# Kernel tuning notes

Hardware: AMD Instinct MI355X
Metric: run time of the kernel (lower is better)

The kernel has to match this reference:

```python
import jax, jax.numpy as jnp
import numpy as np

B, S, V, E, H = 512, 256, 128, 128, 512


def setup_inputs() -> dict:
    key = jax.random.key(0)
    ks = jax.random.split(key, 12)
    s = lambda k, shape, fan: jax.random.normal(k, shape, jnp.float32) * (1.0 / np.sqrt(fan))
    return {
        "x": jax.random.randint(ks[0], (B, S), 0, V),
        "emb": s(ks[1], (V, E), E),
        "Wih0": s(ks[2], (E, H), E),
        "bih0": s(ks[3], (H,), H),
        "Whh0": s(ks[4], (H, H), H),
        "bhh0": s(ks[5], (H,), H),
        "Wih1": s(ks[6], (H, H), H),
        "bih1": s(ks[7], (H,), H),
        "Whh1": s(ks[8], (H, H), H),
        "bhh1": s(ks[9], (H,), H),
        "Wout": s(ks[10], (H, V), H),
        "bout": s(ks[11], (V,), V),
    }


def reference(x, emb, Wih0, bih0, Whh0, bhh0, Wih1, bih1, Whh1, bhh1, Wout, bout):
    # x: [B,S] int -> embedded [B,S,E]
    embedded = emb[x]
    xs = jnp.transpose(embedded, (1, 0, 2))  # [S,B,E] for time-major scan
    h0 = jnp.zeros((x.shape[0], Whh0.shape[0]), embedded.dtype)
    h1 = jnp.zeros((x.shape[0], Whh1.shape[0]), embedded.dtype)

    def step(carry, x_t):
        h0, h1 = carry
        h0 = jnp.tanh(x_t @ Wih0 + bih0 + h0 @ Whh0 + bhh0)
        h1 = jnp.tanh(h0 @ Wih1 + bih1 + h1 @ Whh1 + bhh1)
        return (h0, h1), h1

    _, hs = jax.lax.scan(step, (h0, h1), xs)  # hs: [S,B,H]
    logits = jnp.einsum("sbh,hv->sbv", hs, Wout) + bout
    return jnp.transpose(logits, (1, 0, 2))  # [B,S,V]
```

## Files before the change

### kernel.cpp

```cpp
#include <hip/hip_runtime.h>
#include <hip/hip_bf16.h>


#define Bb 512
#define Ss 256
#define Vv 128
#define Ee 128
#define Hh 512

typedef _Float16 f16;
typedef __attribute__((ext_vector_type(8))) _Float16 f16x8;
typedef __attribute__((ext_vector_type(4))) float f32x4;

#define OFF_H0   0u
#define OFF_H1   2097152u
#define OFF_W0T  4194304u
#define OFF_W1T  4849664u
#define OFF_WOT  5898240u
#define OFF_EMB  6029312u
#define OFF_FLAG 6062080u
#define OFF_CTR  6063104u
#define WS_TOTAL 6063168u

__device__ __forceinline__ f16x8 ld8(const f16* p) {
    return *reinterpret_cast<const f16x8*>(p);
}
#define INV_L1() asm volatile("buffer_inv sc0" ::: "memory")
#define MFMA16(a, b, c) __builtin_amdgcn_mfma_f32_16x16x32_f16((a), (b), (c), 0, 0, 0)

__global__ void prep_kernel(const float* __restrict__ Wih0, const float* __restrict__ Whh0,
                            const float* __restrict__ Wih1, const float* __restrict__ Whh1,
                            const float* __restrict__ Wout, const float* __restrict__ emb,
                            char* __restrict__ ws)
{
    f16* w0t = (f16*)(ws + OFF_W0T);
    f16* w1t = (f16*)(ws + OFF_W1T);
    f16* wot = (f16*)(ws + OFF_WOT);
    f16* e16 = (f16*)(ws + OFF_EMB);
    const int N0 = 512 * 640, N1 = 512 * 1024, N2 = 128 * 512, NE = 128 * 128;
    int i = blockIdx.x * blockDim.x + threadIdx.x;
    if (i < N0) {
        int c = i / 640, k = i - c * 640;
        w0t[i] = (f16)((k < 128) ? Wih0[k * 512 + c] : Whh0[(k - 128) * 512 + c]);
    } else if (i < N0 + N1) {
        int j = i - N0;
        int c = j >> 10, k = j & 1023;
        w1t[j] = (f16)((k < 512) ? Wih1[k * 512 + c] : Whh1[(k - 512) * 512 + c]);
    } else if (i < N0 + N1 + N2) {
        int j = i - (N0 + N1);
        int v = j >> 9, k = j & 511;
        wot[j] = (f16)(Wout[k * 128 + v]);
    } else if (i < N0 + N1 + N2 + NE) {
        int j = i - (N0 + N1 + N2);
        e16[j] = (f16)(emb[j]);
    }
}

__global__ __launch_bounds__(512, 2)
void rnn_kernel(
    const int* __restrict__ x,
    const float* __restrict__ bih0, const float* __restrict__ bhh0,
    const float* __restrict__ bih1, const float* __restrict__ bhh1,
    const float* __restrict__ bout, float* __restrict__ out,
    f16* __restrict__ h0buf, f16* __restrict__ h1buf,
    const f16* __restrict__ w0t, const f16* __restrict__ w1t,
    const f16* __restrict__ wot, const f16* __restrict__ e16,
    int* __restrict__ flags, int* __restrict__ xcdctr)
{
    const int tid = threadIdx.x;

    __shared__ int sslot[2];
    if (tid == 0) {
        unsigned int xcc;
        asm volatile("s_getreg_b32 %0, hwreg(20, 0, 4)" : "=s"(xcc));
        int s = atomicAdd(&xcdctr[xcc & 15], 1);
        sslot[0] = (int)(xcc & 15);
        sslot[1] = s;
    }
    __syncthreads();
    const int xcd = sslot[0], slot = sslot[1];
    const int grp = xcd * 2 + (slot >> 4);
    const int sub = slot & 15;
    const int stg = sub >> 3;
    const int jc  = sub & 7;
    if (grp >= 16) return;
    const int row0 = grp * 32;
    const int col0 = jc * 64;

    int* gflags = flags + grp * 16;

    __shared__ int tok[32];
    __shared__ float bs[64];

    const int lane = tid & 63;
    const int wv = tid >> 6;
    const int mt = wv >> 2, nt = wv & 3;
    const int ar = lane & 15;
    const int kg8 = (lane >> 4) << 3;
    const int arow = row0 + mt * 16 + ar;
    const int crow = row0 + mt * 16 + ((lane >> 4) << 2);
    const int ccol = col0 + nt * 16 + ar;

    if (tid < 64) {
        bs[tid] = (stg == 0) ? (bih0[col0 + tid] + bhh0[col0 + tid])
                             : (bih1[col0 + tid] + bhh1[col0 + tid]);
    }
    __syncthreads();
    const float cbias = bs[nt * 16 + ar];

    if (stg == 0) {
        f16x8 bfr[20];
        {
            const f16* wp = w0t + ccol * 640 + kg8;
            #pragma unroll
            for (int kc = 0; kc < 20; ++kc) bfr[kc] = ld8(wp + kc * 32);
            #pragma unroll
            for (int kc = 0; kc < 20; ++kc) asm volatile("" : "+v"(bfr[kc]));
        }
        const int vcol = jc * 16 + ar;
        const float pbias = bout[vcol];
        const f16* pwb = wot + vcol * Hh + kg8;
        const int prow_base = row0 + mt * 16;

        for (int t = 0; t < Ss; ++t) {
            if (tid >= 64 && tid < 96) tok[tid - 64] = x[(row0 + tid - 64) * Ss + t];
            if (tid < 16) {
                const int tgt = (tid < 8) ? t : (t - 3);
                int it = 0;
                while (__hip_atomic_load(&gflags[tid], __ATOMIC_RELAXED, __HIP_MEMORY_SCOPE_AGENT) < tgt) {
                    if (++it > (1 << 18)) break;
                    __builtin_amdgcn_s_sleep(1);
                }
            }
            __syncthreads();
            INV_L1();
            f16x8 ef[4];
            const f16* ea = e16 + tok[mt * 16 + ar] * Ee + kg8;
            #pragma unroll
            for (int kc = 0; kc < 4; ++kc) ef[kc] = ld8(ea + kc * 32);
            f16x8 hf[16];
            const f16* ha = h0buf + ((t + 3) & 3) * (Bb * Hh) + arow * Hh + kg8;
            #pragma unroll
            for (int kc = 0; kc < 16; ++kc) hf[kc] = ld8(ha + kc * 32);
            f32x4 a0 = {0.f,0.f,0.f,0.f}, a1 = a0, a2 = a0, a3 = a0;
            a0 = MFMA16(ef[0], bfr[0], a0); a1 = MFMA16(ef[1], bfr[1], a1);
            a2 = MFMA16(ef[2], bfr[2], a2); a3 = MFMA16(ef[3], bfr[3], a3);
            #pragma unroll
            for (int kc = 0; kc < 16; kc += 4) {
                a0 = MFMA16(hf[kc + 0], bfr[4 + kc + 0], a0);
                a1 = MFMA16(hf[kc + 1], bfr[4 + kc + 1], a1);
                a2 = MFMA16(hf[kc + 2], bfr[4 + kc + 2], a2);
                a3 = MFMA16(hf[kc + 3], bfr[4 + kc + 3], a3);
            }
            f32x4 acc = (a0 + a1) + (a2 + a3);
            f16* ho = h0buf + (t & 3) * (Bb * Hh) + crow * Hh + ccol;
            #pragma unroll
            for (int i = 0; i < 4; ++i) ho[i * Hh] = (f16)(tanhf(acc[i] + cbias));
            if (t >= 4 && (wv & 3) == (t & 3)) {
                const int tp = t - 4;
                f16x8 pf[16];
                const f16* pa = h1buf + (tp & 3) * (Bb * Hh) + (prow_base + ar) * Hh + kg8;
                #pragma unroll
                for (int kc = 0; kc < 16; ++kc) pf[kc] = ld8(pa + kc * 32);
                f32x4 p0 = {0.f,0.f,0.f,0.f}, p1 = p0, p2 = p0, p3 = p0;
                #pragma unroll
                for (int kc = 0; kc < 16; kc += 4) {
                    p0 = MFMA16(pf[kc + 0], ld8(pwb + (kc + 0) * 32), p0);
                    p1 = MFMA16(pf[kc + 1], ld8(pwb + (kc + 1) * 32), p1);
                    p2 = MFMA16(pf[kc + 2], ld8(pwb + (kc + 2) * 32), p2);
                    p3 = MFMA16(pf[kc + 3], ld8(pwb + (kc + 3) * 32), p3);
                }
                f32x4 pr = (p0 + p1) + (p2 + p3);
                float* op = out + (size_t)(prow_base + ((lane >> 4) << 2)) * (Ss * Vv) + tp * Vv + vcol;
                #pragma unroll
                for (int i = 0; i < 4; ++i) op[i * (Ss * Vv)] = pr[i] + pbias;
            }
            __syncthreads();
            if (tid == 0)
                __hip_atomic_store(&gflags[jc], t + 1, __ATOMIC_RELAXED, __HIP_MEMORY_SCOPE_AGENT);
        }
        if (tid < 8) {
            int it = 0;
            while (__hip_atomic_load(&gflags[8 + tid], __ATOMIC_RELAXED, __HIP_MEMORY_SCOPE_AGENT) < Ss) {
                if (++it > (1 << 18)) break;
                __builtin_amdgcn_s_sleep(1);
            }
        }
        __syncthreads();
        INV_L1();
        {
            const int tp = 252 + (wv & 3);
            f16x8 pf[16];
            const f16* pa = h1buf + (tp & 3) * (Bb * Hh) + (prow_base + ar) * Hh + kg8;
            #pragma unroll
            for (int kc = 0; kc < 16; ++kc) pf[kc] = ld8(pa + kc * 32);
            f32x4 p0 = {0.f,0.f,0.f,0.f}, p1 = p0, p2 = p0, p3 = p0;
            #pragma unroll
            for (int kc = 0; kc < 16; kc += 4) {
                p0 = MFMA16(pf[kc + 0], ld8(pwb + (kc + 0) * 32), p0);
                p1 = MFMA16(pf[kc + 1], ld8(pwb + (kc + 1) * 32), p1);
                p2 = MFMA16(pf[kc + 2], ld8(pwb + (kc + 2) * 32), p2);
                p3 = MFMA16(pf[kc + 3], ld8(pwb + (kc + 3) * 32), p3);
            }
            f32x4 pr = (p0 + p1) + (p2 + p3);
            float* op = out + (size_t)(prow_base + ((lane >> 4) << 2)) * (Ss * Vv) + tp * Vv + vcol;
            #pragma unroll
            for (int i = 0; i < 4; ++i) op[i * (Ss * Vv)] = pr[i] + pbias;
        }
    } else {
        f16x8 bfr[32];
        {
            const f16* wp = w1t + ccol * 1024 + kg8;
            #pragma unroll
            for (int kc = 0; kc < 32; ++kc) bfr[kc] = ld8(wp + kc * 32);
            #pragma unroll
            for (int kc = 0; kc < 32; ++kc) asm volatile("" : "+v"(bfr[kc]));
        }
        for (int t = 0; t < Ss; ++t) {
            if (tid < 16) {
                const int tgt = (tid < 8) ? (t + 1) : t;
                int it = 0;
                while (__hip_atomic_load(&gflags[tid], __ATOMIC_RELAXED, __HIP_MEMORY_SCOPE_AGENT) < tgt) {
                    if (++it > (1 << 18)) break;
                    __builtin_amdgcn_s_sleep(1);
                }
            }
            __syncthreads();
            INV_L1();
            f32x4 a0 = {0.f,0.f,0.f,0.f}, a1 = a0, a2 = a0, a3 = a0;
            {
                f16x8 hf[16];
                const f16* h0a = h0buf + (t & 3) * (Bb * Hh) + arow * Hh + kg8;
                #pragma unroll
                for (int kc = 0; kc < 16; ++kc) hf[kc] = ld8(h0a + kc * 32);
                #pragma unroll
                for (int kc = 0; kc < 16; kc += 4) {
                    a0 = MFMA16(hf[kc + 0], bfr[kc + 0], a0);
                    a1 = MFMA16(hf[kc + 1], bfr[kc + 1], a1);
                    a2 = MFMA16(hf[kc + 2], bfr[kc + 2], a2);
                    a3 = MFMA16(hf[kc + 3], bfr[kc + 3], a3);
                }
            }
            {
                f16x8 hf[16];
                const f16* h1a = h1buf + ((t + 3) & 3) * (Bb * Hh) + arow * Hh + kg8;
                #pragma unroll
                for (int kc = 0; kc < 16; ++kc) hf[kc] = ld8(h1a + kc * 32);
                #pragma unroll
                for (int kc = 0; kc < 16; kc += 4) {
                    a0 = MFMA16(hf[kc + 0], bfr[16 + kc + 0], a0);
                    a1 = MFMA16(hf[kc + 1], bfr[16 + kc + 1], a1);
                    a2 = MFMA16(hf[kc + 2], bfr[16 + kc + 2], a2);
                    a3 = MFMA16(hf[kc + 3], bfr[16 + kc + 3], a3);
                }
            }
            f32x4 acc = (a0 + a1) + (a2 + a3);
            f16* ho = h1buf + (t & 3) * (Bb * Hh) + crow * Hh + ccol;
            #pragma unroll
            for (int i = 0; i < 4; ++i) ho[i * Hh] = (f16)(tanhf(acc[i] + cbias));
            __syncthreads();
            if (tid == 0)
                __hip_atomic_store(&gflags[8 + jc], t + 1, __ATOMIC_RELAXED, __HIP_MEMORY_SCOPE_AGENT);
        }
    }
}

extern "C" void kernel_launch(void* const* d_in, const int* in_sizes, int n_in,
                              void* d_out, int out_size, void* d_ws, size_t ws_size,
                              hipStream_t stream) {
    const int*   x    = (const int*)d_in[0];
    const float* emb  = (const float*)d_in[1];
    const float* Wih0 = (const float*)d_in[2];
    const float* bih0 = (const float*)d_in[3];
    const float* Whh0 = (const float*)d_in[4];
    const float* bhh0 = (const float*)d_in[5];
    const float* Wih1 = (const float*)d_in[6];
    const float* bih1 = (const float*)d_in[7];
    const float* Whh1 = (const float*)d_in[8];
    const float* bhh1 = (const float*)d_in[9];
    const float* Wout = (const float*)d_in[10];
    const float* bout = (const float*)d_in[11];
    float* out = (float*)d_out;
    char*  ws  = (char*)d_ws;

    hipMemsetAsync(d_ws, 0, WS_TOTAL, stream);

    {
        const int total = 512 * 640 + 512 * 1024 + 128 * 512 + 128 * 128;
        prep_kernel<<<(total + 1023) / 1024, 1024, 0, stream>>>(Wih0, Whh0, Wih1, Whh1, Wout, emb, ws);
    }

    f16* h0buf = (f16*)(ws + OFF_H0);
    f16* h1buf = (f16*)(ws + OFF_H1);
    f16* w0t   = (f16*)(ws + OFF_W0T);
    f16* w1t   = (f16*)(ws + OFF_W1T);
    f16* wot   = (f16*)(ws + OFF_WOT);
    f16* e16   = (f16*)(ws + OFF_EMB);
    int* flags = (int*)(ws + OFF_FLAG);
    int* ctr   = (int*)(ws + OFF_CTR);

    void* args[] = { (void*)&x, (void*)&bih0, (void*)&bhh0, (void*)&bih1, (void*)&bhh1,
                     (void*)&bout, (void*)&out, (void*)&h0buf, (void*)&h1buf,
                     (void*)&w0t, (void*)&w1t, (void*)&wot, (void*)&e16,
                     (void*)&flags, (void*)&ctr };
    hipLaunchCooperativeKernel((void*)rnn_kernel, dim3(256), dim3(512), args, 0, stream);
}
```

Before: 2.362 ms.

## Stage RNN weights in LDS and coalesce hidden-state writes via LDS staging

Moves the per-block weight slices (W0, W1, Wout, embedding table) from registers and global memory into padded LDS buffers that are read as MFMA fragments each step. Hidden-state outputs are first staged in LDS and then written to global memory as coalesced 8-byte atomic stores, followed by an explicit vmcnt wait before the flag is published. The L1 invalidate is changed to sc1 scope with a preceding wait. This frees registers (the occupancy hint drops to 1 block per CU) and cuts scattered 2-byte global stores, at the cost of LDS reads in the inner loop and an extra barrier per timestep.

```diff
diff --git a/kernel.cpp b/kernel.cpp
--- a/kernel.cpp
+++ b/kernel.cpp
@@ -22,10 +22,22 @@
 #define OFF_CTR  6063104u
 #define WS_TOTAL 6063168u
 
+#define L_WO   82944
+#define L_EMB  99584
+#define ST_W0  1296
+#define ST_WO  1040
+#define ST_EM  272
+#define ST_W1  2064
+#define L_HS   134400
+#define LDS_BYTES 138496
+
 __device__ __forceinline__ f16x8 ld8(const f16* p) {
     return *reinterpret_cast<const f16x8*>(p);
 }
-#define INV_L1() asm volatile("buffer_inv sc0" ::: "memory")
+__device__ __forceinline__ f16x8 lds_frag(const char* lds, int rowByte, int kElem) {
+    return *reinterpret_cast<const f16x8*>(lds + rowByte + kElem * 2);
+}
+#define INV_L1() asm volatile("s_waitcnt vmcnt(0)\n\tbuffer_inv sc1" ::: "memory")
 #define MFMA16(a, b, c) __builtin_amdgcn_mfma_f32_16x16x32_f16((a), (b), (c), 0, 0, 0)
 
 __global__ void prep_kernel(const float* __restrict__ Wih0, const float* __restrict__ Whh0,
@@ -56,7 +68,7 @@
     }
 }
 
-__global__ __launch_bounds__(512, 2)
+__global__ __launch_bounds__(512)
 void rnn_kernel(
     const int* __restrict__ x,
     const float* __restrict__ bih0, const float* __restrict__ bhh0,
@@ -67,9 +79,10 @@
     const f16* __restrict__ wot, const f16* __restrict__ e16,
     int* __restrict__ flags, int* __restrict__ xcdctr)
 {
+    static __shared__ __attribute__((aligned(16))) char lds[LDS_BYTES];
     const int tid = threadIdx.x;
 
-    __shared__ int sslot[2];
+    __shared__ __attribute__((aligned(16))) int sslot[4];
     if (tid == 0) {
         unsigned int xcc;
         asm volatile("s_getreg_b32 %0, hwreg(20, 0, 4)" : "=s"(xcc));
@@ -89,8 +102,8 @@
 
     int* gflags = flags + grp * 16;
 
-    __shared__ int tok[32];
-    __shared__ float bs[64];
+    __shared__ __attribute__((aligned(16))) int tok[32];
+    __shared__ __attribute__((aligned(16))) float bs[64];
 
     const int lane = tid & 63;
     const int wv = tid >> 6;
@@ -98,28 +111,41 @@
     const int ar = lane & 15;
     const int kg8 = (lane >> 4) << 3;
     const int arow = row0 + mt * 16 + ar;
-    const int crow = row0 + mt * 16 + ((lane >> 4) << 2);
-    const int ccol = col0 + nt * 16 + ar;
-
+    const int cB   = nt * 16 + ar;
+    const int rloc = mt * 16 + ((lane >> 4) << 2);
+
+    if (stg == 0) {
+        for (int i = tid; i < 5120; i += 512) {
+            int c = i / 80, kc = i - c * 80;
+            *(f16x8*)(lds + c * ST_W0 + kc * 16) = ld8(w0t + (col0 + c) * 640 + kc * 8);
+        }
+        for (int i = tid; i < 1024; i += 512) {
+            int r = i >> 6, kc = i & 63;
+            *(f16x8*)(lds + L_WO + r * ST_WO + kc * 16) = ld8(wot + (jc * 16 + r) * 512 + kc * 8);
+        }
+        for (int i = tid; i < 2048; i += 512) {
+            int r = i >> 4, kc = i & 15;
+            *(f16x8*)(lds + L_EMB + r * ST_EM + kc * 16) = ld8(e16 + r * 128 + kc * 8);
+        }
+    } else {
+        for (int i = tid; i < 8192; i += 512) {
+            int c = i >> 7, kc = i & 127;
+            *(f16x8*)(lds + c * ST_W1 + kc * 16) = ld8(w1t + (col0 + c) * 1024 + kc * 8);
+        }
+    }
     if (tid < 64) {
         bs[tid] = (stg == 0) ? (bih0[col0 + tid] + bhh0[col0 + tid])
                              : (bih1[col0 + tid] + bhh1[col0 + tid]);
     }
     __syncthreads();
-    const float cbias = bs[nt * 16 + ar];
+    const float cbias = bs[cB];
+    f16* hstg = (f16*)(lds + L_HS);
 
     if (stg == 0) {
-        f16x8 bfr[20];
-        {
-            const f16* wp = w0t + ccol * 640 + kg8;
-            #pragma unroll
-            for (int kc = 0; kc < 20; ++kc) bfr[kc] = ld8(wp + kc * 32);
-            #pragma unroll
-            for (int kc = 0; kc < 20; ++kc) asm volatile("" : "+v"(bfr[kc]));
-        }
+        const int w0Row = cB * ST_W0;
         const int vcol = jc * 16 + ar;
         const float pbias = bout[vcol];
-        const f16* pwb = wot + vcol * Hh + kg8;
+        const int woRow = L_WO + ar * ST_WO;
         const int prow_base = row0 + mt * 16;
 
         for (int t = 0; t < Ss; ++t) {
@@ -134,28 +160,33 @@
             }
             __syncthreads();
             INV_L1();
-            f16x8 ef[4];
-            const f16* ea = e16 + tok[mt * 16 + ar] * Ee + kg8;
-            #pragma unroll
-            for (int kc = 0; kc < 4; ++kc) ef[kc] = ld8(ea + kc * 32);
+            const int myTok = tok[mt * 16 + ar];
+            const int embRow = L_EMB + myTok * ST_EM;
             f16x8 hf[16];
             const f16* ha = h0buf + ((t + 3) & 3) * (Bb * Hh) + arow * Hh + kg8;
             #pragma unroll
             for (int kc = 0; kc < 16; ++kc) hf[kc] = ld8(ha + kc * 32);
             f32x4 a0 = {0.f,0.f,0.f,0.f}, a1 = a0, a2 = a0, a3 = a0;
-            a0 = MFMA16(ef[0], bfr[0], a0); a1 = MFMA16(ef[1], bfr[1], a1);
-            a2 = MFMA16(ef[2], bfr[2], a2); a3 = MFMA16(ef[3], bfr[3], a3);
-            #pragma unroll
-            for (int kc = 0; kc < 16; kc += 4) {
-                a0 = MFMA16(hf[kc + 0], bfr[4 + kc + 0], a0);
-                a1 = MFMA16(hf[kc + 1], bfr[4 + kc + 1], a1);
-                a2 = MFMA16(hf[kc + 2], bfr[4 + kc + 2], a2);
-                a3 = MFMA16(hf[kc + 3], bfr[4 + kc + 3], a3);
+            #pragma unroll
+            for (int kc = 0; kc < 4; ++kc) {
+                f16x8 af = lds_frag(lds, embRow, kc * 32 + kg8);
+                f16x8 bw = lds_frag(lds, w0Row, kc * 32 + kg8);
+                if ((kc & 3) == 0) a0 = MFMA16(af, bw, a0);
+                else if ((kc & 3) == 1) a1 = MFMA16(af, bw, a1);
+                else if ((kc & 3) == 2) a2 = MFMA16(af, bw, a2);
+                else a3 = MFMA16(af, bw, a3);
+            }
+            #pragma unroll
+            for (int kc = 0; kc < 16; ++kc) {
+                f16x8 bw = lds_frag(lds, w0Row, 128 + kc * 32 + kg8);
+                if ((kc & 3) == 0) a0 = MFMA16(hf[kc], bw, a0);
+                else if ((kc & 3) == 1) a1 = MFMA16(hf[kc], bw, a1);
+                else if ((kc & 3) == 2) a2 = MFMA16(hf[kc], bw, a2);
+                else a3 = MFMA16(hf[kc], bw, a3);
             }
             f32x4 acc = (a0 + a1) + (a2 + a3);
-            f16* ho = h0buf + (t & 3) * (Bb * Hh) + crow * Hh + ccol;
-            #pragma unroll
-            for (int i = 0; i < 4; ++i) ho[i * Hh] = (f16)(tanhf(acc[i] + cbias));
+            #pragma unroll
+            for (int i = 0; i < 4; ++i) hstg[(rloc + i) * 64 + cB] = (f16)(tanhf(acc[i] + cbias));
             if (t >= 4 && (wv & 3) == (t & 3)) {
                 const int tp = t - 4;
                 f16x8 pf[16];
@@ -165,16 +196,24 @@
                 f32x4 p0 = {0.f,0.f,0.f,0.f}, p1 = p0, p2 = p0, p3 = p0;
                 #pragma unroll
                 for (int kc = 0; kc < 16; kc += 4) {
-                    p0 = MFMA16(pf[kc + 0], ld8(pwb + (kc + 0) * 32), p0);
-                    p1 = MFMA16(pf[kc + 1], ld8(pwb + (kc + 1) * 32), p1);
-                    p2 = MFMA16(pf[kc + 2], ld8(pwb + (kc + 2) * 32), p2);
-                    p3 = MFMA16(pf[kc + 3], ld8(pwb + (kc + 3) * 32), p3);
+                    p0 = MFMA16(pf[kc + 0], lds_frag(lds, woRow, (kc + 0) * 32 + kg8), p0);
+                    p1 = MFMA16(pf[kc + 1], lds_frag(lds, woRow, (kc + 1) * 32 + kg8), p1);
+                    p2 = MFMA16(pf[kc + 2], lds_frag(lds, woRow, (kc + 2) * 32 + kg8), p2);
+                    p3 = MFMA16(pf[kc + 3], lds_frag(lds, woRow, (kc + 3) * 32 + kg8), p3);
                 }
                 f32x4 pr = (p0 + p1) + (p2 + p3);
                 float* op = out + (size_t)(prow_base + ((lane >> 4) << 2)) * (Ss * Vv) + tp * Vv + vcol;
                 #pragma unroll
                 for (int i = 0; i < 4; ++i) op[i * (Ss * Vv)] = pr[i] + pbias;
             }
+            __syncthreads();
+            {
+                unsigned long long v = ((const unsigned long long*)hstg)[tid];
+                unsigned long long* hg = (unsigned long long*)(h0buf + (t & 3) * (Bb * Hh)
+                                            + (row0 + (tid >> 4)) * Hh + col0 + ((tid & 15) << 2));
+                __hip_atomic_store(hg, v, __ATOMIC_RELAXED, __HIP_MEMORY_SCOPE_AGENT);
+            }
+            asm volatile("s_waitcnt vmcnt(0)" ::: "memory");
             __syncthreads();
             if (tid == 0)
                 __hip_atomic_store(&gflags[jc], t + 1, __ATOMIC_RELAXED, __HIP_MEMORY_SCOPE_AGENT);
@@ -197,10 +236,10 @@
             f32x4 p0 = {0.f,0.f,0.f,0.f}, p1 = p0, p2 = p0, p3 = p0;
             #pragma unroll
             for (int kc = 0; kc < 16; kc += 4) {
-                p0 = MFMA16(pf[kc + 0], ld8(pwb + (kc + 0) * 32), p0);
-                p1 = MFMA16(pf[kc + 1], ld8(pwb + (kc + 1) * 32), p1);
-                p2 = MFMA16(pf[kc + 2], ld8(pwb + (kc + 2) * 32), p2);
-                p3 = MFMA16(pf[kc + 3], ld8(pwb + (kc + 3) * 32), p3);
+                p0 = MFMA16(pf[kc + 0], lds_frag(lds, woRow, (kc + 0) * 32 + kg8), p0);
+                p1 = MFMA16(pf[kc + 1], lds_frag(lds, woRow, (kc + 1) * 32 + kg8), p1);
+                p2 = MFMA16(pf[kc + 2], lds_frag(lds, woRow, (kc + 2) * 32 + kg8), p2);
+                p3 = MFMA16(pf[kc + 3], lds_frag(lds, woRow, (kc + 3) * 32 + kg8), p3);
             }
             f32x4 pr = (p0 + p1) + (p2 + p3);
             float* op = out + (size_t)(prow_base + ((lane >> 4) << 2)) * (Ss * Vv) + tp * Vv + vcol;
@@ -208,14 +247,7 @@
             for (int i = 0; i < 4; ++i) op[i * (Ss * Vv)] = pr[i] + pbias;
         }
     } else {
-        f16x8 bfr[32];
-        {
-            const f16* wp = w1t + ccol * 1024 + kg8;
-            #pragma unroll
-            for (int kc = 0; kc < 32; ++kc) bfr[kc] = ld8(wp + kc * 32);
-            #pragma unroll
-            for (int kc = 0; kc < 32; ++kc) asm volatile("" : "+v"(bfr[kc]));
-        }
+        const int w1Row = cB * ST_W1;
         for (int t = 0; t < Ss; ++t) {
             if (tid < 16) {
                 const int tgt = (tid < 8) ? (t + 1) : t;
@@ -227,37 +259,39 @@
             }
             __syncthreads();
             INV_L1();
+            f16x8 hf[16], gf[16];
+            const f16* h0a = h0buf + (t & 3) * (Bb * Hh) + arow * Hh + kg8;
+            const f16* h1a = h1buf + ((t + 3) & 3) * (Bb * Hh) + arow * Hh + kg8;
+            #pragma unroll
+            for (int kc = 0; kc < 16; ++kc) hf[kc] = ld8(h0a + kc * 32);
+            #pragma unroll
+            for (int kc = 0; kc < 16; ++kc) gf[kc] = ld8(h1a + kc * 32);
             f32x4 a0 = {0.f,0.f,0.f,0.f}, a1 = a0, a2 = a0, a3 = a0;
+            #pragma unroll
+            for (int kc = 0; kc < 16; kc += 4) {
+                a0 = MFMA16(hf[kc + 0], lds_frag(lds, w1Row, (kc + 0) * 32 + kg8), a0);
+                a1 = MFMA16(hf[kc + 1], lds_frag(lds, w1Row, (kc + 1) * 32 + kg8), a1);
+                a2 = MFMA16(hf[kc + 2], lds_frag(lds, w1Row, (kc + 2) * 32 + kg8), a2);
+                a3 = MFMA16(hf[kc + 3], lds_frag(lds, w1Row, (kc + 3) * 32 + kg8), a3);
+            }
+            #pragma unroll
+            for (int kc = 0; kc < 16; kc += 4) {
+                a0 = MFMA16(gf[kc + 0], lds_frag(lds, w1Row, 512 + (kc + 0) * 32 + kg8), a0);
+                a1 = MFMA16(gf[kc + 1], lds_frag(lds, w1Row, 512 + (kc + 1) * 32 + kg8), a1);
+                a2 = MFMA16(gf[kc + 2], lds_frag(lds, w1Row, 512 + (kc + 2) * 32 + kg8), a2);
+                a3 = MFMA16(gf[kc + 3], lds_frag(lds, w1Row, 512 + (kc + 3) * 32 + kg8), a3);
+            }
+            f32x4 acc = (a0 + a1) + (a2 + a3);
+            #pragma unroll
+            for (int i = 0; i < 4; ++i) hstg[(rloc + i) * 64 + cB] = (f16)(tanhf(acc[i] + cbias));
+            __syncthreads();
             {
-                f16x8 hf[16];
-                const f16* h0a = h0buf + (t & 3) * (Bb * Hh) + arow * Hh + kg8;
-                #pragma unroll
-                for (int kc = 0; kc < 16; ++kc) hf[kc] = ld8(h0a + kc * 32);
-                #pragma unroll
-                for (int kc = 0; kc < 16; kc += 4) {
-                    a0 = MFMA16(hf[kc + 0], bfr[kc + 0], a0);
-                    a1 = MFMA16(hf[kc + 1], bfr[kc + 1], a1);
-                    a2 = MFMA16(hf[kc + 2], bfr[kc + 2], a2);
-                    a3 = MFMA16(hf[kc + 3], bfr[kc + 3], a3);
-                }
-            }
-            {
-                f16x8 hf[16];
-                const f16* h1a = h1buf + ((t + 3) & 3) * (Bb * Hh) + arow * Hh + kg8;
-                #pragma unroll
-                for (int kc = 0; kc < 16; ++kc) hf[kc] = ld8(h1a + kc * 32);
-                #pragma unroll
-                for (int kc = 0; kc < 16; kc += 4) {
-                    a0 = MFMA16(hf[kc + 0], bfr[16 + kc + 0], a0);
-                    a1 = MFMA16(hf[kc + 1], bfr[16 + kc + 1], a1);
-                    a2 = MFMA16(hf[kc + 2], bfr[16 + kc + 2], a2);
-                    a3 = MFMA16(hf[kc + 3], bfr[16 + kc + 3], a3);
-                }
-            }
-            f32x4 acc = (a0 + a1) + (a2 + a3);
-            f16* ho = h1buf + (t & 3) * (Bb * Hh) + crow * Hh + ccol;
-            #pragma unroll
-            for (int i = 0; i < 4; ++i) ho[i * Hh] = (f16)(tanhf(acc[i] + cbias));
+                unsigned long long v = ((const unsigned long long*)hstg)[tid];
+                unsigned long long* hg = (unsigned long long*)(h1buf + (t & 3) * (Bb * Hh)
+                                            + (row0 + (tid >> 4)) * Hh + col0 + ((tid & 15) << 2));
+                __hip_atomic_store(hg, v, __ATOMIC_RELAXED, __HIP_MEMORY_SCOPE_AGENT);
+            }
+            asm volatile("s_waitcnt vmcnt(0)" ::: "memory");
             __syncthreads();
             if (tid == 0)
                 __hip_atomic_store(&gflags[8 + jc], t + 1, __ATOMIC_RELAXED, __HIP_MEMORY_SCOPE_AGENT);
```

After: 4.557 ms. 1.93x slower.
